# Kernel tuning notes

Measured on AMD Instinct MI355X. Metric: run time of the kernel, lower is better.

The kernel has to match this reference:

```python
import jax, jax.numpy as jnp
import numpy as np

THRESHOLD = 0.5
NEG_POS_RATIO = 3
ALPHA = 1.0
B, P, C, O = 128, 8732, 21, 32


def xy_to_cxcy(xy):
    return jnp.concatenate([(xy[..., 2:] + xy[..., :2]) / 2, xy[..., 2:] - xy[..., :2]], axis=-1)


def cxcy_to_xy(cxcy):
    return jnp.concatenate([cxcy[..., :2] - cxcy[..., 2:] / 2, cxcy[..., :2] + cxcy[..., 2:] / 2], axis=-1)


def cxcy_to_gcxgcy(cxcy, priors_cxcy):
    g_cxcy = (cxcy[..., :2] - priors_cxcy[..., :2]) / (priors_cxcy[..., 2:] / 10.0)
    g_wh = jnp.log(cxcy[..., 2:] / priors_cxcy[..., 2:]) * 5.0
    return jnp.concatenate([g_cxcy, g_wh], axis=-1)


def find_jaccard_overlap(set1, set2):
    # set1: [O,4] xy, set2: [P,4] xy -> [O,P]
    lo = jnp.maximum(set1[:, None, :2], set2[None, :, :2])
    hi = jnp.minimum(set1[:, None, 2:], set2[None, :, 2:])
    inter = jnp.prod(jnp.clip(hi - lo, 0.0), axis=-1)
    a1 = jnp.prod(set1[:, 2:] - set1[:, :2], axis=-1)
    a2 = jnp.prod(set2[:, 2:] - set2[:, :2], axis=-1)
    union = a1[:, None] + a2[None, :] - inter
    return inter / union


def setup_inputs() -> dict:
    key = jax.random.key(0)
    k0, k1, k2, k3, k4, k5, k6 = jax.random.split(key, 7)
    predicted_locs = jax.random.normal(k0, (B, P, 4), jnp.float32)
    predicted_scores = jax.random.normal(k1, (B, P, C), jnp.float32)
    centers = jax.random.uniform(k2, (B, O, 2), jnp.float32, 0.2, 0.8)
    sizes = jax.random.uniform(k3, (B, O, 2), jnp.float32, 0.05, 0.3)
    boxes = jnp.concatenate([centers - sizes / 2, centers + sizes / 2], axis=-1)
    labels = jax.random.randint(k4, (B, O), 0, C)
    p_c = jax.random.uniform(k5, (P, 2), jnp.float32, 0.05, 0.95)
    p_wh = jax.random.uniform(k6, (P, 2), jnp.float32, 0.05, 0.5)
    priors_cxcy = jnp.concatenate([p_c, p_wh], axis=-1)
    return {"predicted_locs": predicted_locs, "predicted_scores": predicted_scores,
            "boxes": boxes, "labels": labels, "priors_cxcy": priors_cxcy}


def reference(predicted_locs, predicted_scores, boxes, labels, priors_cxcy):
    priors_xy = cxcy_to_xy(priors_cxcy)

    def match_one(boxes_i, labels_i):
        overlap = find_jaccard_overlap(boxes_i, priors_xy)           # [O,P]
        overlap_for_each_prior = jnp.max(overlap, axis=0)            # [P]
        object_for_each_prior = jnp.argmax(overlap, axis=0)          # [P]
        prior_for_each_object = jnp.argmax(overlap, axis=1)          # [O]
        object_for_each_prior = object_for_each_prior.at[prior_for_each_object].set(jnp.arange(O))
        overlap_for_each_prior = overlap_for_each_prior.at[prior_for_each_object].set(1.0)
        label_for_each_prior = labels_i[object_for_each_prior]
        label_for_each_prior = jnp.where(overlap_for_each_prior < THRESHOLD, 0, label_for_each_prior)
        true_locs_i = cxcy_to_gcxgcy(xy_to_cxcy(boxes_i[object_for_each_prior]), priors_cxcy)
        return label_for_each_prior, true_locs_i

    true_classes, true_locs = jax.vmap(match_one)(boxes, labels)     # [B,P], [B,P,4]

    positive = true_classes != 0                                     # [B,P]
    n_positives = jnp.sum(positive, axis=1)                          # [B]
    n_pos_total = jnp.sum(n_positives)

    # L1Loss (mean over selected positive elements, 4 per prior)
    abs_diff = jnp.abs(predicted_locs - true_locs)                   # [B,P,4]
    loc_loss = jnp.sum(abs_diff * positive[..., None]) / (n_pos_total.astype(jnp.float32) * 4.0)

    # per-element cross-entropy
    log_p = jax.nn.log_softmax(predicted_scores, axis=-1)            # [B,P,C]
    conf_loss_all = -jnp.take_along_axis(log_p, true_classes[..., None], axis=-1)[..., 0]  # [B,P]

    conf_loss_pos_sum = jnp.sum(jnp.where(positive, conf_loss_all, 0.0))
    conf_loss_neg = jnp.where(positive, 0.0, conf_loss_all)
    conf_loss_neg_sorted = -jnp.sort(-conf_loss_neg, axis=1)         # descending
    n_hard = NEG_POS_RATIO * n_positives                             # [B]
    hard_mask = jnp.arange(P)[None, :] < n_hard[:, None]             # [B,P]
    conf_loss_hard_neg_sum = jnp.sum(jnp.where(hard_mask, conf_loss_neg_sorted, 0.0))

    conf_loss = (conf_loss_hard_neg_sum + conf_loss_pos_sum) / n_pos_total.astype(jnp.float32)
    return conf_loss + ALPHA * loc_loss
```

## Files before the change

### kernel.cpp

```cpp
#include <hip/hip_runtime.h>

#define NB 128
#define NP 8732
#define NO 32
#define NC 21
#define NCHUNK 35


__device__ __forceinline__ float wave64_fmax_u(float m) {
    int v;
    v = __builtin_amdgcn_update_dpp(__float_as_int(m), __float_as_int(m), 0x111, 0xf, 0xf, false);
    m = fmaxf(m, __int_as_float(v));
    v = __builtin_amdgcn_update_dpp(__float_as_int(m), __float_as_int(m), 0x112, 0xf, 0xf, false);
    m = fmaxf(m, __int_as_float(v));
    v = __builtin_amdgcn_update_dpp(__float_as_int(m), __float_as_int(m), 0x114, 0xf, 0xf, false);
    m = fmaxf(m, __int_as_float(v));
    v = __builtin_amdgcn_update_dpp(__float_as_int(m), __float_as_int(m), 0x118, 0xf, 0xf, false);
    m = fmaxf(m, __int_as_float(v));
    v = __builtin_amdgcn_update_dpp(__float_as_int(m), __float_as_int(m), 0x142, 0xf, 0xf, false);
    m = fmaxf(m, __int_as_float(v));
    v = __builtin_amdgcn_update_dpp(__float_as_int(m), __float_as_int(m), 0x143, 0xf, 0xf, false);
    m = fmaxf(m, __int_as_float(v));
    return __int_as_float(__builtin_amdgcn_readlane(__float_as_int(m), 63));
}

__device__ __forceinline__ int wave64_imin_u(int m) {
    int v;
    v = __builtin_amdgcn_update_dpp(m, m, 0x111, 0xf, 0xf, false); m = v < m ? v : m;
    v = __builtin_amdgcn_update_dpp(m, m, 0x112, 0xf, 0xf, false); m = v < m ? v : m;
    v = __builtin_amdgcn_update_dpp(m, m, 0x114, 0xf, 0xf, false); m = v < m ? v : m;
    v = __builtin_amdgcn_update_dpp(m, m, 0x118, 0xf, 0xf, false); m = v < m ? v : m;
    v = __builtin_amdgcn_update_dpp(m, m, 0x142, 0xf, 0xf, false); m = v < m ? v : m;
    v = __builtin_amdgcn_update_dpp(m, m, 0x143, 0xf, 0xf, false); m = v < m ? v : m;
    return __builtin_amdgcn_readlane(m, 63);
}

__global__ __launch_bounds__(256) void k_obj(const float* __restrict__ boxes,
                                             const float* __restrict__ priors,
                                             int* __restrict__ pfor) {
    __shared__ unsigned long long part[4][4];
    int b = blockIdx.y;
    int tid = threadIdx.x, lane = tid & 63, wid = tid >> 6;
    int o0 = blockIdx.x * 4;

    float4 bx[4]; float a1[4];
#pragma unroll
    for (int i = 0; i < 4; ++i) {
        bx[i] = ((const float4*)boxes)[b * NO + o0 + i];
        a1[i] = (bx[i].z - bx[i].x) * (bx[i].w - bx[i].y);
    }

    float bv[4]; int bp[4];
#pragma unroll
    for (int i = 0; i < 4; ++i) { bv[i] = 0.0f; bp[i] = tid; }
    const float4* pr4 = (const float4*)priors;

    for (int k = 0; k < 34; ++k) {
        int p = tid + (k << 8);
        float4 pr = pr4[p];
        float x1 = pr.x - pr.z * 0.5f, y1 = pr.y - pr.w * 0.5f;
        float x2 = pr.x + pr.z * 0.5f, y2 = pr.y + pr.w * 0.5f;
        float pa = (x2 - x1) * (y2 - y1);
#pragma unroll
        for (int i = 0; i < 4; ++i) {
            float lx = fmaxf(bx[i].x, x1), ly = fmaxf(bx[i].y, y1);
            float hx = fminf(bx[i].z, x2), hy = fminf(bx[i].w, y2);
            float inter = fmaxf(hx - lx, 0.0f) * fmaxf(hy - ly, 0.0f);
            if (__ballot(inter > 0.0f)) {
                float iou = inter / (a1[i] + pa - inter);
                if (iou > bv[i]) { bv[i] = iou; bp[i] = p; }
            }
        }
    }
    {
        int p = tid + 8704;
        if (p < NP) {
            float4 pr = pr4[p];
            float x1 = pr.x - pr.z * 0.5f, y1 = pr.y - pr.w * 0.5f;
            float x2 = pr.x + pr.z * 0.5f, y2 = pr.y + pr.w * 0.5f;
            float pa = (x2 - x1) * (y2 - y1);
#pragma unroll
            for (int i = 0; i < 4; ++i) {
                float lx = fmaxf(bx[i].x, x1), ly = fmaxf(bx[i].y, y1);
                float hx = fminf(bx[i].z, x2), hy = fminf(bx[i].w, y2);
                float inter = fmaxf(hx - lx, 0.0f) * fmaxf(hy - ly, 0.0f);
                if (__ballot(inter > 0.0f)) {
                    float iou = inter / (a1[i] + pa - inter);
                    if (iou > bv[i]) { bv[i] = iou; bp[i] = p; }
                }
            }
        }
    }

#pragma unroll
    for (int i = 0; i < 4; ++i) {
        float m = wave64_fmax_u(bv[i]);
        int mp = wave64_imin_u((bv[i] == m) ? bp[i] : 0x7FFFFFFF);
        if (lane == 0)
            part[wid][i] = ((unsigned long long)__float_as_uint(m) << 32) |
                           (unsigned long long)(0xFFFFFFFFu - (unsigned)mp);
    }
    __syncthreads();
    if (tid < 4) {
        unsigned long long best = part[0][tid];
        if (part[1][tid] > best) best = part[1][tid];
        if (part[2][tid] > best) best = part[2][tid];
        if (part[3][tid] > best) best = part[3][tid];
        pfor[b * NO + o0 + tid] = (int)(0xFFFFFFFFu - (unsigned)(best & 0xFFFFFFFFull));
    }
}

__global__ __launch_bounds__(256) void k_loss(const float* __restrict__ plocs,
                                              const float* __restrict__ scores,
                                              const float* __restrict__ boxes,
                                              const int* __restrict__ labels,
                                              const float* __restrict__ priors,
                                              const int* __restrict__ pfor,
                                              float* __restrict__ confneg,
                                              int* __restrict__ pnp,
                                              double* __restrict__ pd0,
                                              double* __restrict__ pd1,
                                              int* __restrict__ donecnt) {
    __shared__ float4 sbox[NO];
    __shared__ float  sa1[NO];
    __shared__ int    slbl[NO];
    __shared__ int    sfp[NO], sfo[NO];
    __shared__ int    snf;
    int b = blockIdx.y;
    int p0 = blockIdx.x * 256;
    int tid = threadIdx.x;

    if (tid < NO) {
        float4 bxx = ((const float4*)boxes)[b * NO + tid];
        sbox[tid] = bxx;
        sa1[tid]  = (bxx.z - bxx.x) * (bxx.w - bxx.y);
        slbl[tid] = labels[b * NO + tid];
    }
    if (tid < 64) {
        int f = -1, inr = 0;
        if (tid < NO) {
            f = pfor[b * NO + tid];
            inr = (f >= p0) && (f < p0 + 256);
        }
        unsigned long long mask = __ballot(inr);
        if (inr) {
            int rank = __popcll(mask & ((1ull << tid) - 1));
            sfp[rank] = f; sfo[rank] = tid;
        }
        if (tid == 0) snf = __popcll(mask);
    }
    __syncthreads();

    int p = p0 + tid;
    float posconf = 0.0f, locpart = 0.0f;
    int isp = 0;

    if (p < NP) {
        float4 pr = ((const float4*)priors)[p];
        float px1 = pr.x - pr.z * 0.5f, py1 = pr.y - pr.w * 0.5f;
        float px2 = pr.x + pr.z * 0.5f, py2 = pr.y + pr.w * 0.5f;
        float pa  = (px2 - px1) * (py2 - py1);

        float bestv = 0.0f; int besto = 0;
#pragma unroll
        for (int o = 0; o < NO; ++o) {
            float4 bxx = sbox[o];
            float lx = fmaxf(bxx.x, px1), ly = fmaxf(bxx.y, py1);
            float hx = fminf(bxx.z, px2), hy = fminf(bxx.w, py2);
            float inter = fmaxf(hx - lx, 0.0f) * fmaxf(hy - ly, 0.0f);
            if (__ballot(inter > 0.0f)) {
                float iou = inter / (sa1[o] + pa - inter);
                if (iou > bestv) { bestv = iou; besto = o; }
            }
        }
        int obj = besto;
        int mat = bestv >= 0.5f ? 1 : 0;
        int nf = snf;
        for (int i = 0; i < nf; ++i)
            if (sfp[i] == p) { obj = sfo[i]; mat = 1; }
        int lbl = mat ? slbl[obj] : 0;

        const float* srow = scores + ((size_t)b * NP + p) * NC;
        const float4* r4 = (const float4*)srow;
        float4 q0 = r4[0], q1 = r4[1], q2 = r4[2], q3 = r4[3], q4 = r4[4];
        float sl = srow[lbl];

        float s[NC] = {q0.x, q0.y, q0.z, q0.w, q1.x, q1.y, q1.z, q1.w,
                       q2.x, q2.y, q2.z, q2.w, q3.x, q3.y, q3.z, q3.w,
                       q4.x, q4.y, q4.z, q4.w, srow[20]};
        float m = s[0];
#pragma unroll
        for (int c = 1; c < NC; ++c) m = fmaxf(m, s[c]);
        float sum = 0.0f;
#pragma unroll
        for (int c = 0; c < NC; ++c) sum += __expf(s[c] - m);
        float conf = m + __logf(sum) - sl;

        if (lbl != 0) {
            isp = 1;
            posconf = conf;
            float4 bxx = sbox[obj];
            float cx = (bxx.x + bxx.z) * 0.5f, cy = (bxx.y + bxx.w) * 0.5f;
            float w = bxx.z - bxx.x, h = bxx.w - bxx.y;
            float gx = (cx - pr.x) / (pr.z * 0.1f);
            float gy = (cy - pr.y) / (pr.w * 0.1f);
            float gw = __logf(w / pr.z) * 5.0f;
            float gh = __logf(h / pr.w) * 5.0f;
            float4 pl = ((const float4*)plocs)[(size_t)b * NP + p];
            locpart = fabsf(pl.x - gx) + fabsf(pl.y - gy) +
                      fabsf(pl.z - gw) + fabsf(pl.w - gh);
        }
        confneg[(size_t)b * NP + p] = isp ? 0.0f : conf;
    }

    for (int s = 32; s > 0; s >>= 1) {
        posconf += __shfl_xor(posconf, s, 64);
        locpart += __shfl_xor(locpart, s, 64);
        isp     += __shfl_xor(isp, s, 64);
    }
    __shared__ float w0[4], w1[4];
    __shared__ int wc[4];
    int wid = tid >> 6, lane = tid & 63;
    if (lane == 0) { w0[wid] = posconf; w1[wid] = locpart; wc[wid] = isp; }
    __syncthreads();
    if (tid == 0) {
        int pb = b * NCHUNK + blockIdx.x;
        pd0[pb] = (double)(w0[0] + w0[1] + w0[2] + w0[3]);
        pd1[pb] = (double)(w1[0] + w1[1] + w1[2] + w1[3]);
        pnp[pb] = wc[0] + wc[1] + wc[2] + wc[3];
        if (pb == 0) *donecnt = 0;
    }
}

__global__ __launch_bounds__(1024) void k_topk(const float* __restrict__ confneg,
                                               const int* __restrict__ pnp,
                                               const double* __restrict__ pd0,
                                               const double* __restrict__ pd1,
                                               int* __restrict__ snp,
                                               double* __restrict__ sums,
                                               int* __restrict__ donecnt,
                                               float* __restrict__ out) {
    __shared__ unsigned long long sq[2][16];
    __shared__ int    siw[16];
    __shared__ double sdd[16];
    __shared__ int    sk;
    int tid = threadIdx.x, b = blockIdx.x;
    int lane = tid & 63, wid = tid >> 6;

    if (wid == 0) {
        int np_ = 0; double d0 = 0.0, d1 = 0.0;
        if (lane < NCHUNK) {
            int pb = b * NCHUNK + lane;
            np_ = pnp[pb]; d0 = pd0[pb]; d1 = pd1[pb];
        }
        for (int s = 32; s > 0; s >>= 1) {
            np_ += __shfl_xor(np_, s, 64);
            d0  += __shfl_xor(d0, s, 64);
            d1  += __shfl_xor(d1, s, 64);
        }
        if (lane == 0) {
            int k = np_ * 3; if (k > NP) k = NP;
            sk = k;
            snp[b] = np_;
            sums[b * 3 + 1] = d0;
            sums[b * 3 + 2] = d1;
        }
    }

    const float* src = confneg + (size_t)b * NP;
    float val[9];
#pragma unroll
    for (int j = 0; j < 9; ++j) {
        int i = tid + j * 1024;
        val[j] = (i < NP) ? src[i] : 0.0f;
    }
    __syncthreads();
    int k = sk;

    double hn = 0.0;
    if (k > 0) {
        unsigned T = 0;
        int par = 0;
        {
            unsigned cand = 1u << 30;
            int cnt = 0;
#pragma unroll
            for (int j = 0; j < 9; ++j)
                cnt += __popcll(__ballot(__float_as_uint(val[j]) >= cand));
            if (lane == 0) sq[par][wid] = (unsigned long long)cnt;
            __syncthreads();
            unsigned long long t = 0;
#pragma unroll
            for (int w = 0; w < 16; ++w) t += sq[par][w];
            par ^= 1;
            if ((int)t >= k) T = cand;
        }
        for (int sh = 28; sh >= 0; sh -= 2) {
            unsigned c1 = T | (1u << sh), c2 = T | (2u << sh), c3 = T | (3u << sh);
            int n1 = 0, n2 = 0, n3 = 0;
#pragma unroll
            for (int j = 0; j < 9; ++j) {
                unsigned u = __float_as_uint(val[j]);
                n1 += __popcll(__ballot(u >= c1));
                n2 += __popcll(__ballot(u >= c2));
                n3 += __popcll(__ballot(u >= c3));
            }
            if (lane == 0)
                sq[par][wid] = (unsigned long long)n1 |
                               ((unsigned long long)n2 << 20) |
                               ((unsigned long long)n3 << 40);
            __syncthreads();
            unsigned long long t = 0;
#pragma unroll
            for (int w = 0; w < 16; ++w) t += sq[par][w];
            par ^= 1;
            int t1 = (int)(t & 0xFFFFF), t2 = (int)((t >> 20) & 0xFFFFF),
                t3 = (int)((t >> 40) & 0xFFFFF);
            if      (t3 >= k) T = c3;
            else if (t2 >= k) T = c2;
            else if (t1 >= k) T = c1;
        }

        int cgt = 0;
        double sgt = 0.0;
#pragma unroll
        for (int j = 0; j < 9; ++j) {
            unsigned u = __float_as_uint(val[j]);
            if (u > T) { cgt++; sgt += (double)val[j]; }
        }
        for (int s = 32; s > 0; s >>= 1) {
            cgt += __shfl_xor(cgt, s, 64);
            sgt += __shfl_xor(sgt, s, 64);
        }
        if (lane == 0) { siw[wid] = cgt; sdd[wid] = sgt; }
        __syncthreads();
        if (tid == 0) {
            int cg = 0; double sg = 0.0;
            for (int w = 0; w < 16; ++w) { cg += siw[w]; sg += sdd[w]; }
            hn = sg + (double)(k - cg) * (double)__uint_as_float(T);
        }
    }
    if (tid == 0) sums[b * 3 + 0] = hn;

    __shared__ int samlast;
    if (tid == 0) {
        __threadfence();
        int prev = atomicAdd(donecnt, 1);
        samlast = (prev == NB - 1) ? 1 : 0;
    }
    __syncthreads();
    if (!samlast) return;
    __threadfence();

    double hnn = 0.0, pc = 0.0, lc = 0.0, npd = 0.0;
    if (tid < NB) {
        hnn = atomicAdd(&sums[tid * 3 + 0], 0.0);
        pc  = atomicAdd(&sums[tid * 3 + 1], 0.0);
        lc  = atomicAdd(&sums[tid * 3 + 2], 0.0);
        npd = (double)atomicAdd((int*)&snp[tid], 0);
    }
    for (int s = 32; s > 0; s >>= 1) {
        hnn += __shfl_xor(hnn, s, 64);
        pc  += __shfl_xor(pc, s, 64);
        lc  += __shfl_xor(lc, s, 64);
        npd += __shfl_xor(npd, s, 64);
    }
    __shared__ double sfin[4][2];
    if (lane == 0 && wid < 2) {
        sfin[0][wid] = hnn; sfin[1][wid] = pc; sfin[2][wid] = lc; sfin[3][wid] = npd;
    }
    __syncthreads();
    if (tid == 0) {
        double H  = sfin[0][0] + sfin[0][1];
        double P  = sfin[1][0] + sfin[1][1];
        double L  = sfin[2][0] + sfin[2][1];
        double nt = sfin[3][0] + sfin[3][1];
        out[0] = (float)((H + P) / nt + L / (nt * 4.0));
    }
}

extern "C" void kernel_launch(void* const* d_in, const int* in_sizes, int n_in,
                              void* d_out, int out_size, void* d_ws, size_t ws_size,
                              hipStream_t stream) {
    const float* plocs  = (const float*)d_in[0];
    const float* scores = (const float*)d_in[1];
    const float* boxes  = (const float*)d_in[2];
    const int*   labels = (const int*)d_in[3];
    const float* priors = (const float*)d_in[4];
    float* out = (float*)d_out;

    char* ws = (char*)d_ws;
    int*    pfor    = (int*)ws;
    double* pd0     = (double*)(ws + 16384);
    double* pd1     = (double*)(ws + 52224);
    int*    pnp     = (int*)(ws + 88064);
    int*    snp     = (int*)(ws + 105984);
    double* sums    = (double*)(ws + 106496);
    int*    donecnt = (int*)(ws + 109568);
    float*  confneg = (float*)(ws + 109824);

    hipLaunchKernelGGL(k_obj, dim3(NO / 4, NB), dim3(256), 0, stream,
                       boxes, priors, pfor);
    hipLaunchKernelGGL(k_loss, dim3(NCHUNK, NB), dim3(256), 0, stream,
                       plocs, scores, boxes, labels, priors, pfor,
                       confneg, pnp, pd0, pd1, donecnt);
    hipLaunchKernelGGL(k_topk, dim3(NB), dim3(1024), 0, stream,
                       confneg, pnp, pd0, pd1, snp, sums, donecnt, out);
}
```

Baseline: 220.1 us.

## Fuse object matching into loss kernel and apply forced-match corrections in tail

Merges the per-object best-prior search into the per-prior loss kernel as extra blocks, so the two run concurrently in one launch instead of serialising across a kernel boundary. Because the loss blocks no longer know the forced prior-object assignments, each prior's tentative match code is written out. The top-k kernel then patches the affected priors, recomputing conf/loc deltas and the confneg entries before the selection. It also drops the ballot-based skip of the IoU divide, which removes a branch but does the divide for every pair. This adds an extra code buffer write and serial fixup work on one wave per batch.

New measurement: 224.4 us. Within noise of the previous version (+2.0%).

```diff
diff --git a/kernel.cpp b/kernel.cpp
--- a/kernel.cpp
+++ b/kernel.cpp
@@ -5,6 +5,7 @@
 #define NO 32
 #define NC 21
 #define NCHUNK 35
+#define NOBLK 8
 
 
 __device__ __forceinline__ float wave64_fmax_u(float m) {
@@ -35,46 +36,38 @@
     return __builtin_amdgcn_readlane(m, 63);
 }
 
-__global__ __launch_bounds__(256) void k_obj(const float* __restrict__ boxes,
-                                             const float* __restrict__ priors,
-                                             int* __restrict__ pfor) {
-    __shared__ unsigned long long part[4][4];
+__global__ __launch_bounds__(256) void k_main(const float* __restrict__ plocs,
+                                              const float* __restrict__ scores,
+                                              const float* __restrict__ boxes,
+                                              const int* __restrict__ labels,
+                                              const float* __restrict__ priors,
+                                              float* __restrict__ confneg,
+                                              int* __restrict__ code,
+                                              int* __restrict__ pnp,
+                                              double* __restrict__ pd0,
+                                              double* __restrict__ pd1,
+                                              int* __restrict__ pfor,
+                                              int* __restrict__ donecnt) {
     int b = blockIdx.y;
     int tid = threadIdx.x, lane = tid & 63, wid = tid >> 6;
-    int o0 = blockIdx.x * 4;
-
-    float4 bx[4]; float a1[4];
-#pragma unroll
-    for (int i = 0; i < 4; ++i) {
-        bx[i] = ((const float4*)boxes)[b * NO + o0 + i];
-        a1[i] = (bx[i].z - bx[i].x) * (bx[i].w - bx[i].y);
-    }
-
-    float bv[4]; int bp[4];
-#pragma unroll
-    for (int i = 0; i < 4; ++i) { bv[i] = 0.0f; bp[i] = tid; }
-    const float4* pr4 = (const float4*)priors;
-
-    for (int k = 0; k < 34; ++k) {
-        int p = tid + (k << 8);
-        float4 pr = pr4[p];
-        float x1 = pr.x - pr.z * 0.5f, y1 = pr.y - pr.w * 0.5f;
-        float x2 = pr.x + pr.z * 0.5f, y2 = pr.y + pr.w * 0.5f;
-        float pa = (x2 - x1) * (y2 - y1);
+
+    if (blockIdx.x >= NCHUNK) {
+        __shared__ unsigned long long part[4][4];
+        int o0 = (blockIdx.x - NCHUNK) * 4;
+
+        float4 bx[4]; float a1[4];
 #pragma unroll
         for (int i = 0; i < 4; ++i) {
-            float lx = fmaxf(bx[i].x, x1), ly = fmaxf(bx[i].y, y1);
-            float hx = fminf(bx[i].z, x2), hy = fminf(bx[i].w, y2);
-            float inter = fmaxf(hx - lx, 0.0f) * fmaxf(hy - ly, 0.0f);
-            if (__ballot(inter > 0.0f)) {
-                float iou = inter / (a1[i] + pa - inter);
-                if (iou > bv[i]) { bv[i] = iou; bp[i] = p; }
-            }
-        }
-    }
-    {
-        int p = tid + 8704;
-        if (p < NP) {
+            bx[i] = ((const float4*)boxes)[b * NO + o0 + i];
+            a1[i] = (bx[i].z - bx[i].x) * (bx[i].w - bx[i].y);
+        }
+        float bv[4]; int bp[4];
+#pragma unroll
+        for (int i = 0; i < 4; ++i) { bv[i] = 0.0f; bp[i] = tid; }
+        const float4* pr4 = (const float4*)priors;
+
+        for (int k = 0; k < 34; ++k) {
+            int p = tid + (k << 8);
             float4 pr = pr4[p];
             float x1 = pr.x - pr.z * 0.5f, y1 = pr.y - pr.w * 0.5f;
             float x2 = pr.x + pr.z * 0.5f, y2 = pr.y + pr.w * 0.5f;
@@ -84,51 +77,50 @@
                 float lx = fmaxf(bx[i].x, x1), ly = fmaxf(bx[i].y, y1);
                 float hx = fminf(bx[i].z, x2), hy = fminf(bx[i].w, y2);
                 float inter = fmaxf(hx - lx, 0.0f) * fmaxf(hy - ly, 0.0f);
-                if (__ballot(inter > 0.0f)) {
+                float iou = inter / (a1[i] + pa - inter);
+                if (iou > bv[i]) { bv[i] = iou; bp[i] = p; }
+            }
+        }
+        {
+            int p = tid + 8704;
+            if (p < NP) {
+                float4 pr = pr4[p];
+                float x1 = pr.x - pr.z * 0.5f, y1 = pr.y - pr.w * 0.5f;
+                float x2 = pr.x + pr.z * 0.5f, y2 = pr.y + pr.w * 0.5f;
+                float pa = (x2 - x1) * (y2 - y1);
+#pragma unroll
+                for (int i = 0; i < 4; ++i) {
+                    float lx = fmaxf(bx[i].x, x1), ly = fmaxf(bx[i].y, y1);
+                    float hx = fminf(bx[i].z, x2), hy = fminf(bx[i].w, y2);
+                    float inter = fmaxf(hx - lx, 0.0f) * fmaxf(hy - ly, 0.0f);
                     float iou = inter / (a1[i] + pa - inter);
                     if (iou > bv[i]) { bv[i] = iou; bp[i] = p; }
                 }
             }
         }
-    }
-
-#pragma unroll
-    for (int i = 0; i < 4; ++i) {
-        float m = wave64_fmax_u(bv[i]);
-        int mp = wave64_imin_u((bv[i] == m) ? bp[i] : 0x7FFFFFFF);
-        if (lane == 0)
-            part[wid][i] = ((unsigned long long)__float_as_uint(m) << 32) |
-                           (unsigned long long)(0xFFFFFFFFu - (unsigned)mp);
-    }
-    __syncthreads();
-    if (tid < 4) {
-        unsigned long long best = part[0][tid];
-        if (part[1][tid] > best) best = part[1][tid];
-        if (part[2][tid] > best) best = part[2][tid];
-        if (part[3][tid] > best) best = part[3][tid];
-        pfor[b * NO + o0 + tid] = (int)(0xFFFFFFFFu - (unsigned)(best & 0xFFFFFFFFull));
-    }
-}
-
-__global__ __launch_bounds__(256) void k_loss(const float* __restrict__ plocs,
-                                              const float* __restrict__ scores,
-                                              const float* __restrict__ boxes,
-                                              const int* __restrict__ labels,
-                                              const float* __restrict__ priors,
-                                              const int* __restrict__ pfor,
-                                              float* __restrict__ confneg,
-                                              int* __restrict__ pnp,
-                                              double* __restrict__ pd0,
-                                              double* __restrict__ pd1,
-                                              int* __restrict__ donecnt) {
+#pragma unroll
+        for (int i = 0; i < 4; ++i) {
+            float m = wave64_fmax_u(bv[i]);
+            int mp = wave64_imin_u((bv[i] == m) ? bp[i] : 0x7FFFFFFF);
+            if (lane == 0)
+                part[wid][i] = ((unsigned long long)__float_as_uint(m) << 32) |
+                               (unsigned long long)(0xFFFFFFFFu - (unsigned)mp);
+        }
+        __syncthreads();
+        if (tid < 4) {
+            unsigned long long best = part[0][tid];
+            if (part[1][tid] > best) best = part[1][tid];
+            if (part[2][tid] > best) best = part[2][tid];
+            if (part[3][tid] > best) best = part[3][tid];
+            pfor[b * NO + o0 + tid] = (int)(0xFFFFFFFFu - (unsigned)(best & 0xFFFFFFFFull));
+        }
+        return;
+    }
+
     __shared__ float4 sbox[NO];
     __shared__ float  sa1[NO];
     __shared__ int    slbl[NO];
-    __shared__ int    sfp[NO], sfo[NO];
-    __shared__ int    snf;
-    int b = blockIdx.y;
     int p0 = blockIdx.x * 256;
-    int tid = threadIdx.x;
 
     if (tid < NO) {
         float4 bxx = ((const float4*)boxes)[b * NO + tid];
@@ -136,19 +128,6 @@
         sa1[tid]  = (bxx.z - bxx.x) * (bxx.w - bxx.y);
         slbl[tid] = labels[b * NO + tid];
     }
-    if (tid < 64) {
-        int f = -1, inr = 0;
-        if (tid < NO) {
-            f = pfor[b * NO + tid];
-            inr = (f >= p0) && (f < p0 + 256);
-        }
-        unsigned long long mask = __ballot(inr);
-        if (inr) {
-            int rank = __popcll(mask & ((1ull << tid) - 1));
-            sfp[rank] = f; sfo[rank] = tid;
-        }
-        if (tid == 0) snf = __popcll(mask);
-    }
     __syncthreads();
 
     int p = p0 + tid;
@@ -168,17 +147,12 @@
             float lx = fmaxf(bxx.x, px1), ly = fmaxf(bxx.y, py1);
             float hx = fminf(bxx.z, px2), hy = fminf(bxx.w, py2);
             float inter = fmaxf(hx - lx, 0.0f) * fmaxf(hy - ly, 0.0f);
-            if (__ballot(inter > 0.0f)) {
-                float iou = inter / (sa1[o] + pa - inter);
-                if (iou > bestv) { bestv = iou; besto = o; }
-            }
-        }
-        int obj = besto;
+            float iou = inter / (sa1[o] + pa - inter);
+            if (iou > bestv) { bestv = iou; besto = o; }
+        }
         int mat = bestv >= 0.5f ? 1 : 0;
-        int nf = snf;
-        for (int i = 0; i < nf; ++i)
-            if (sfp[i] == p) { obj = sfo[i]; mat = 1; }
-        int lbl = mat ? slbl[obj] : 0;
+        int lbl = mat ? slbl[besto] : 0;
+        code[(size_t)b * NP + p] = besto | (mat << 8);
 
         const float* srow = scores + ((size_t)b * NP + p) * NC;
         const float4* r4 = (const float4*)srow;
@@ -199,7 +173,7 @@
         if (lbl != 0) {
             isp = 1;
             posconf = conf;
-            float4 bxx = sbox[obj];
+            float4 bxx = sbox[besto];
             float cx = (bxx.x + bxx.z) * 0.5f, cy = (bxx.y + bxx.w) * 0.5f;
             float w = bxx.z - bxx.x, h = bxx.w - bxx.y;
             float gx = (cx - pr.x) / (pr.z * 0.1f);
@@ -220,7 +194,6 @@
     }
     __shared__ float w0[4], w1[4];
     __shared__ int wc[4];
-    int wid = tid >> 6, lane = tid & 63;
     if (lane == 0) { w0[wid] = posconf; w1[wid] = locpart; wc[wid] = isp; }
     __syncthreads();
     if (tid == 0) {
@@ -232,7 +205,14 @@
     }
 }
 
-__global__ __launch_bounds__(1024) void k_topk(const float* __restrict__ confneg,
+__global__ __launch_bounds__(1024) void k_tail(const float* __restrict__ plocs,
+                                               const float* __restrict__ scores,
+                                               const float* __restrict__ boxes,
+                                               const int* __restrict__ labels,
+                                               const float* __restrict__ priors,
+                                               const int* __restrict__ pfor,
+                                               const int* __restrict__ code,
+                                               float* __restrict__ confneg,
                                                const int* __restrict__ pnp,
                                                const double* __restrict__ pd0,
                                                const double* __restrict__ pd1,
@@ -244,11 +224,12 @@
     __shared__ int    siw[16];
     __shared__ double sdd[16];
     __shared__ int    sk;
+    __shared__ int    sfp[NO];
     int tid = threadIdx.x, b = blockIdx.x;
     int lane = tid & 63, wid = tid >> 6;
 
+    int np_ = 0; double d0 = 0.0, d1 = 0.0;
     if (wid == 0) {
-        int np_ = 0; double d0 = 0.0, d1 = 0.0;
         if (lane < NCHUNK) {
             int pb = b * NCHUNK + lane;
             np_ = pnp[pb]; d0 = pd0[pb]; d1 = pd1[pb];
@@ -258,6 +239,74 @@
             d0  += __shfl_xor(d0, s, 64);
             d1  += __shfl_xor(d1, s, 64);
         }
+        if (lane < NO) sfp[lane] = pfor[b * NO + lane];
+    }
+    __syncthreads();
+
+    if (wid == 0) {
+        int dnp = 0; double dpos = 0.0, dloc = 0.0;
+        if (lane < NO) {
+            int p = sfp[lane];
+            bool winner = true;
+            for (int o2 = lane + 1; o2 < NO; ++o2)
+                if (sfp[o2] == p) winner = false;
+            if (winner) {
+                int cd = code[(size_t)b * NP + p];
+                int obj_old = cd & 255, mat_old = cd >> 8;
+                if (!(mat_old && obj_old == (int)lane)) {
+                    int lbl_old = mat_old ? labels[b * NO + obj_old] : 0;
+                    int lbl_new = labels[b * NO + lane];
+                    const float* srow = scores + ((size_t)b * NP + p) * NC;
+                    float s[NC];
+#pragma unroll
+                    for (int c = 0; c < NC; ++c) s[c] = srow[c];
+                    float m = s[0];
+#pragma unroll
+                    for (int c = 1; c < NC; ++c) m = fmaxf(m, s[c]);
+                    float sum = 0.0f;
+#pragma unroll
+                    for (int c = 0; c < NC; ++c) sum += __expf(s[c] - m);
+                    float conf_old = m + __logf(sum) - srow[lbl_old];
+                    float conf_new = m + __logf(sum) - srow[lbl_new];
+                    int io = lbl_old != 0, in_ = lbl_new != 0;
+                    dnp  = in_ - io;
+                    dpos = (in_ ? (double)conf_new : 0.0) - (io ? (double)conf_old : 0.0);
+                    float4 pr = ((const float4*)priors)[p];
+                    float4 pl = ((const float4*)plocs)[(size_t)b * NP + p];
+                    float ln = 0.0f, lo = 0.0f;
+                    {
+                        float4 bxx = ((const float4*)boxes)[b * NO + lane];
+                        float cx = (bxx.x + bxx.z) * 0.5f, cy = (bxx.y + bxx.w) * 0.5f;
+                        float w = bxx.z - bxx.x, h = bxx.w - bxx.y;
+                        float gx = (cx - pr.x) / (pr.z * 0.1f);
+                        float gy = (cy - pr.y) / (pr.w * 0.1f);
+                        float gw = __logf(w / pr.z) * 5.0f;
+                        float gh = __logf(h / pr.w) * 5.0f;
+                        ln = fabsf(pl.x - gx) + fabsf(pl.y - gy) +
+                             fabsf(pl.z - gw) + fabsf(pl.w - gh);
+                    }
+                    if (io) {
+                        float4 bxx = ((const float4*)boxes)[b * NO + obj_old];
+                        float cx = (bxx.x + bxx.z) * 0.5f, cy = (bxx.y + bxx.w) * 0.5f;
+                        float w = bxx.z - bxx.x, h = bxx.w - bxx.y;
+                        float gx = (cx - pr.x) / (pr.z * 0.1f);
+                        float gy = (cy - pr.y) / (pr.w * 0.1f);
+                        float gw = __logf(w / pr.z) * 5.0f;
+                        float gh = __logf(h / pr.w) * 5.0f;
+                        lo = fabsf(pl.x - gx) + fabsf(pl.y - gy) +
+                             fabsf(pl.z - gw) + fabsf(pl.w - gh);
+                    }
+                    dloc = (in_ ? (double)ln : 0.0) - (io ? (double)lo : 0.0);
+                    confneg[(size_t)b * NP + p] = in_ ? 0.0f : conf_new;
+                }
+            }
+        }
+        for (int s = 32; s > 0; s >>= 1) {
+            dnp  += __shfl_xor(dnp, s, 64);
+            dpos += __shfl_xor(dpos, s, 64);
+            dloc += __shfl_xor(dloc, s, 64);
+        }
+        np_ += dnp; d0 += dpos; d1 += dloc;
         if (lane == 0) {
             int k = np_ * 3; if (k > NP) k = NP;
             sk = k;
@@ -266,6 +315,8 @@
             sums[b * 3 + 2] = d1;
         }
     }
+    __threadfence_block();
+    __syncthreads();
 
     const float* src = confneg + (size_t)b * NP;
     float val[9];
@@ -274,7 +325,6 @@
         int i = tid + j * 1024;
         val[j] = (i < NP) ? src[i] : 0.0f;
     }
-    __syncthreads();
     int k = sk;
 
     double hn = 0.0;
@@ -398,12 +448,12 @@
     double* sums    = (double*)(ws + 106496);
     int*    donecnt = (int*)(ws + 109568);
     float*  confneg = (float*)(ws + 109824);
-
-    hipLaunchKernelGGL(k_obj, dim3(NO / 4, NB), dim3(256), 0, stream,
-                       boxes, priors, pfor);
-    hipLaunchKernelGGL(k_loss, dim3(NCHUNK, NB), dim3(256), 0, stream,
-                       plocs, scores, boxes, labels, priors, pfor,
-                       confneg, pnp, pd0, pd1, donecnt);
-    hipLaunchKernelGGL(k_topk, dim3(NB), dim3(1024), 0, stream,
+    int*    code    = (int*)(ws + 4580608);
+
+    hipLaunchKernelGGL(k_main, dim3(NCHUNK + NOBLK, NB), dim3(256), 0, stream,
+                       plocs, scores, boxes, labels, priors,
+                       confneg, code, pnp, pd0, pd1, pfor, donecnt);
+    hipLaunchKernelGGL(k_tail, dim3(NB), dim3(1024), 0, stream,
+                       plocs, scores, boxes, labels, priors, pfor, code,
                        confneg, pnp, pd0, pd1, snp, sums, donecnt, out);
 }
```
